# Optimization experiments

Measured on AMD Instinct MI355X. Metric: run time of the kernel, lower is better.

## Reference

```python
import jax, jax.numpy as jnp
import numpy as np

B, BARS, BEATS, FRAC = 64, 16, 4, 8
IN_F = 10 * 47 * 2  # 940
LIN_OUT = 100
BEAT_H = 16
BAR_H = 32


def _p(key, shape, scale=0.05):
    return jax.random.normal(key, shape, dtype=jnp.float32) * scale


def setup_inputs() -> dict:
    key = jax.random.key(0)
    ks = jax.random.split(key, 16)
    return {
        "channels": jax.random.normal(ks[0], (B, BARS, BEATS, FRAC, 10, 2, 47), dtype=jnp.float32),
        "lin_w": _p(ks[1], (LIN_OUT, IN_F)),
        "lin_b": _p(ks[2], (LIN_OUT,)),
        # beats LSTM (unidirectional), PyTorch gate order i,f,g,o
        "b_wih": _p(ks[3], (4 * BEAT_H, LIN_OUT)),
        "b_whh": _p(ks[4], (4 * BEAT_H, BEAT_H)),
        "b_bih": _p(ks[5], (4 * BEAT_H,)),
        "b_bhh": _p(ks[6], (4 * BEAT_H,)),
        # bars LSTM, bidirectional: forward (f_) and reverse (r_) directions
        "f_wih": _p(ks[7], (4 * BAR_H, BEAT_H)),
        "f_whh": _p(ks[8], (4 * BAR_H, BAR_H)),
        "f_bih": _p(ks[9], (4 * BAR_H,)),
        "f_bhh": _p(ks[10], (4 * BAR_H,)),
        "r_wih": _p(ks[11], (4 * BAR_H, BEAT_H)),
        "r_whh": _p(ks[12], (4 * BAR_H, BAR_H)),
        "r_bih": _p(ks[13], (4 * BAR_H,)),
        "r_bhh": _p(ks[14], (4 * BAR_H,)),
    }


def lstm(x, wih, whh, bih, bhh):
    """PyTorch-semantics LSTM, batch_first. x: [N, T, F] -> h_seq [N, T, H]."""
    N = x.shape[0]
    H = whh.shape[1]
    # precompute input contribution for all timesteps
    xg = jnp.einsum('ntf,gf->ntg', x, wih) + (bih + bhh)  # [N, T, 4H]

    def step(carry, xt):
        h, c = carry
        gates = xt + h @ whh.T  # [N, 4H]
        i, f, g, o = jnp.split(gates, 4, axis=-1)
        c = jax.nn.sigmoid(f) * c + jax.nn.sigmoid(i) * jnp.tanh(g)
        h = jax.nn.sigmoid(o) * jnp.tanh(c)
        return (h, c), h

    h0 = jnp.zeros((N, H), x.dtype)
    _, hs = jax.lax.scan(step, (h0, h0), jnp.swapaxes(xg, 0, 1))  # [T, N, H]
    return jnp.swapaxes(hs, 0, 1)


def bilstm(x, f_wih, f_whh, f_bih, f_bhh, r_wih, r_whh, r_bih, r_bhh):
    fwd = lstm(x, f_wih, f_whh, f_bih, f_bhh)
    bwd = jnp.flip(lstm(jnp.flip(x, axis=1), r_wih, r_whh, r_bih, r_bhh), axis=1)
    return jnp.concatenate([fwd, bwd], axis=-1)


def reference(channels, lin_w, lin_b,
              b_wih, b_whh, b_bih, b_bhh,
              f_wih, f_whh, f_bih, f_bhh,
              r_wih, r_whh, r_bih, r_bhh):
    # channels: [B, bars, beats, frac, 10, 2, 47]
    x = jnp.swapaxes(channels, -1, -2)  # [..., 10, 47, 2]
    x = x.reshape(*x.shape[:4], IN_F)   # squash dims 4..6 -> 940
    x = jax.nn.relu(x @ lin_w.T + lin_b)  # [B, bars, beats, frac, 100]

    # Distributed depth=2: fold (B, bars, beats) into batch, seq over frac
    xb = x.reshape(B * BARS * BEATS, FRAC, LIN_OUT)
    beats = lstm(xb, b_wih, b_whh, b_bih, b_bhh)
    beats = beats.reshape(B, BARS, BEATS, FRAC, BEAT_H)

    # last fraction hidden state, then Distributed depth=1 over beats axis
    xl = beats[:, :, :, -1].reshape(B * BARS, BEATS, BEAT_H)
    bars = bilstm(xl, f_wih, f_whh, f_bih, f_bhh, r_wih, r_whh, r_bih, r_bhh)
    bars = bars.reshape(B, BARS, BEATS, 2 * BAR_H)
    return beats, bars
```

## Files before the change

kernel.cpp:

```cpp
#include <hip/hip_runtime.h>
#include <hip/hip_bf16.h>

typedef float f32x4 __attribute__((ext_vector_type(4)));
typedef short bf16x8 __attribute__((ext_vector_type(8)));
typedef short bf16x4 __attribute__((ext_vector_type(4)));

#define MFMA16(a, b, c) __builtin_amdgcn_mfma_f32_16x16x32_bf16(a, b, c, 0, 0, 0)

constexpr int K1  = 940;
constexpr int NP  = 112;
constexpr int OSL = 136;
constexpr int CHE = 14336;
constexpr int CHB = 28672;

__device__ __forceinline__ float sigf(float x) { return 1.f / (1.f + __expf(-x)); }
__device__ __forceinline__ float tanhfast(float x) { return 2.f / (1.f + __expf(-2.f * x)) - 1.f; }

__device__ __forceinline__ short f2b(float x) {
  __hip_bfloat16 b = __float2bfloat16(x);
  return *reinterpret_cast<short*>(&b);
}

__device__ __forceinline__ void gl_lds16(const void* g, void* l) {
  __builtin_amdgcn_global_load_lds(
      (const __attribute__((address_space(1))) unsigned int*)g,
      (__attribute__((address_space(3))) unsigned int*)l, 16, 0, 0);
}

__global__ void prep_kernel(const float* __restrict__ lin_w,
                            const float* __restrict__ b_wih,
                            __hip_bfloat16* __restrict__ w2c,
                            __hip_bfloat16* __restrict__ bw2) {
  int idx = blockIdx.x * 256 + threadIdx.x;
  if (idx < NP * 1024) {
    int n = idx >> 10, k = idx & 1023;
    float v = 0.f;
    if (n < 100 && k < K1) {
      int c10 = k / 94, rem = k - c10 * 94;
      int c2 = rem / 47, c47 = rem - c2 * 47;
      int f = c10 * 94 + c47 * 2 + c2;
      v = lin_w[n * K1 + f];
    }
    int c = k >> 7, kk = k & 127;
    w2c[c * CHE + n * 128 + (kk ^ ((n & 7) << 3))] = __float2bfloat16(v);
  } else {
    int i2 = idx - NP * 1024;
    if (i2 < 64 * 128) {
      int g = i2 >> 7, k = i2 & 127;
      bw2[i2] = __float2bfloat16((k < 100) ? b_wih[g * 100 + k] : 0.f);
    }
  }
}

__global__ __launch_bounds__(256, 2)
void linear_gemm(const float* __restrict__ ch,
                 const __hip_bfloat16* __restrict__ w2c,
                 const float* __restrict__ lin_b,
                 __hip_bfloat16* __restrict__ out1) {
  __shared__ __align__(16) char smem[73728];
  char* As = smem;
  char* Bs = smem + 16384;

  const int tid = threadIdx.x;
  const int w = tid >> 6, lane = tid & 63;
  const int l16 = lane & 15, bq = lane >> 4;
  const int row0 = blockIdx.x * 64 + w * 16;

  float4 rA[8];
  const float4 f40{0.f, 0.f, 0.f, 0.f};
  const int acolf = (lane & 31) * 4;
  const float* asrc = ch + (long)(row0 + (lane >> 5)) * K1 + acolf;
  auto ldA = [&](int c) {
    const float* p = asrc + c * 128;
    if (c < 7) {
#pragma unroll
      for (int j = 0; j < 8; ++j)
        rA[j] = *reinterpret_cast<const float4*>(p + (long)j * 2 * K1);
    } else {
      const bool ok = acolf < 44;
#pragma unroll
      for (int j = 0; j < 8; ++j)
        rA[j] = ok ? *reinterpret_cast<const float4*>(p + (long)j * 2 * K1) : f40;
    }
  };
  auto stA = [&]() {
#pragma unroll
    for (int j = 0; j < 8; ++j) {
      const int row = w * 16 + (lane >> 5) + 2 * j;
      const int byte = row * 256 + (((lane & 31) * 8) ^ ((row & 7) << 4));
      bf16x4 v = {f2b(rA[j].x), f2b(rA[j].y), f2b(rA[j].z), f2b(rA[j].w)};
      *reinterpret_cast<bf16x4*>(As + byte) = v;
    }
  };

  auto dmaB = [&](int c, int buf) {
    const __hip_bfloat16* src = w2c + c * CHE + w * 3584 + lane * 8;
    char* dst = Bs + buf * CHB + w * 7168;
#pragma unroll
    for (int j = 0; j < 7; ++j)
      gl_lds16(src + j * 512, dst + j * 1024);
  };

  ldA(0);
  dmaB(0, 0);
  stA();
  asm volatile("s_waitcnt vmcnt(0) lgkmcnt(0)" ::: "memory");
  __builtin_amdgcn_s_barrier();
  __builtin_amdgcn_sched_barrier(0);

  f32x4 acc[7] = {};
  const int fsw = (l16 & 7) << 4;
  const int abase = (w * 16 + l16) * 256;

#pragma unroll
  for (int c = 0; c < 8; ++c) {
    if (c < 7) {
      ldA(c + 1);
      dmaB(c + 1, (c + 1) & 1);
    }
    const char* Bp = Bs + (c & 1) * CHB;
#pragma unroll
    for (int ks = 0; ks < 4; ++ks) {
      const int ko = (ks * 64 + bq * 16) ^ fsw;
      bf16x8 a = *reinterpret_cast<const bf16x8*>(As + abase + ko);
#pragma unroll
      for (int nt = 0; nt < 7; ++nt) {
        bf16x8 b = *reinterpret_cast<const bf16x8*>(Bp + (nt * 16 + l16) * 256 + ko);
        acc[nt] = MFMA16(a, b, acc[nt]);
      }
    }
    asm volatile("s_waitcnt lgkmcnt(0)" ::: "memory");
    if (c < 7) stA();
    asm volatile("s_waitcnt vmcnt(0) lgkmcnt(0)" ::: "memory");
    __builtin_amdgcn_s_barrier();
    __builtin_amdgcn_sched_barrier(0);
  }

#pragma unroll
  for (int nt = 0; nt < 7; ++nt) {
    const int col = nt * 16 + l16;
    const float bias = (col < 100) ? lin_b[col] : 0.f;
#pragma unroll
    for (int r = 0; r < 4; ++r) {
      float v = (col < 100) ? fmaxf(acc[nt][r] + bias, 0.f) : 0.f;
      out1[(long)(row0 + bq * 4 + r) * 112 + col] = __float2bfloat16(v);
    }
  }
}

__global__ __launch_bounds__(256)
void lstm_kernel(const __hip_bfloat16* __restrict__ out1,
                 const __hip_bfloat16* __restrict__ bw2,
                 const float* __restrict__ bih,
                 const float* __restrict__ bhh,
                 const float* __restrict__ whh,
                 const float* __restrict__ fwih, const float* __restrict__ fwhh,
                 const float* __restrict__ fbih, const float* __restrict__ fbhh,
                 const float* __restrict__ rwih, const float* __restrict__ rwhh,
                 const float* __restrict__ rbih, const float* __restrict__ rbhh,
                 float* __restrict__ beats,
                 float* __restrict__ bars) {
  __shared__ __align__(16) __hip_bfloat16 out_s[64 * OSL];
  __shared__ float xg_s[64 * 65];
  __shared__ float hlast[8][16];
  __shared__ float hb[2][32];
  __shared__ float gact[2][128];

  const int tid = threadIdx.x;
  const int w = tid >> 6, lane = tid & 63;
  const int l16 = lane & 15, bq = lane >> 4;
  const long rbase = (long)blockIdx.x * 64;

#pragma unroll
  for (int it = 0; it < 4; ++it) {
    const int e = it * 256 + tid;
    if (e < 896) {
      const int row = e / 14, g = e - row * 14;
      *reinterpret_cast<bf16x8*>(&out_s[row * OSL + g * 8]) =
          *reinterpret_cast<const bf16x8*>(&out1[(rbase + row) * 112 + g * 8]);
    }
  }
  if (tid < 128) {
    const int row = tid >> 1, c0 = 112 + (tid & 1) * 8;
    bf16x8 z = {0, 0, 0, 0, 0, 0, 0, 0};
    *reinterpret_cast<bf16x8*>(&out_s[row * OSL + c0]) = z;
  }
  __syncthreads();

  {
    bf16x8 av[4];
#pragma unroll
    for (int s = 0; s < 4; ++s)
      av[s] = *reinterpret_cast<const bf16x8*>(&out_s[(w * 16 + l16) * OSL + s * 32 + bq * 8]);
    f32x4 xacc[4] = {};
#pragma unroll
    for (int gt = 0; gt < 4; ++gt) {
#pragma unroll
      for (int s = 0; s < 4; ++s) {
        bf16x8 b = *reinterpret_cast<const bf16x8*>(&bw2[(gt * 16 + l16) * 128 + s * 32 + bq * 8]);
        xacc[gt] = MFMA16(av[s], b, xacc[gt]);
      }
    }
#pragma unroll
    for (int gt = 0; gt < 4; ++gt) {
      const int gate = gt * 16 + l16;
      const float bias = bih[gate] + bhh[gate];
#pragma unroll
      for (int r = 0; r < 4; ++r)
        xg_s[(w * 16 + bq * 4 + r) * 65 + gate] = xacc[gt][r] + bias;
    }
  }

  {
    const int cell = lane & 15;
    float wr[16];
#pragma unroll
    for (int u = 0; u < 16; ++u) wr[u] = whh[lane * 16 + u];
    float xv0[8], xv1[8];
#pragma unroll
    for (int t = 0; t < 8; ++t) {
      xv0[t] = xg_s[(w * 16 + t) * 65 + lane];
      xv1[t] = xg_s[(w * 16 + 8 + t) * 65 + lane];
    }
    float h0[16], h1[16];
#pragma unroll
    for (int u = 0; u < 16; ++u) { h0[u] = 0.f; h1[u] = 0.f; }
    float c0 = 0.f, c1 = 0.f;
    const long sg0 = (long)blockIdx.x * 8 + 2 * w;
    const long sg1 = sg0 + 1;
#pragma unroll
    for (int t = 0; t < 8; ++t) {
      float p0 = xv0[t], p1 = xv1[t];
#pragma unroll
      for (int u = 0; u < 16; ++u) { p0 += wr[u] * h0[u]; p1 += wr[u] * h1[u]; }
      const bool istanh = (lane >= 32 && lane < 48);
      float a0 = istanh ? tanhfast(p0) : sigf(p0);
      float a1 = istanh ? tanhfast(p1) : sigf(p1);
      float gi0 = __shfl(a0, cell),      gi1 = __shfl(a1, cell);
      float gf0 = __shfl(a0, cell + 16), gf1 = __shfl(a1, cell + 16);
      float gg0 = __shfl(a0, cell + 32), gg1 = __shfl(a1, cell + 32);
      float go0 = __shfl(a0, cell + 48), go1 = __shfl(a1, cell + 48);
      c0 = gf0 * c0 + gi0 * gg0;
      c1 = gf1 * c1 + gi1 * gg1;
      float hn0 = go0 * tanhfast(c0);
      float hn1 = go1 * tanhfast(c1);
#pragma unroll
      for (int u = 0; u < 16; ++u) { h0[u] = __shfl(hn0, u); h1[u] = __shfl(hn1, u); }
      if (lane < 16) {
        beats[sg0 * 128 + t * 16 + lane] = hn0;
        beats[sg1 * 128 + t * 16 + lane] = hn1;
        if (t == 7) {
          hlast[2 * w][lane]     = hn0;
          hlast[2 * w + 1][lane] = hn1;
        }
      }
    }
  }
  __syncthreads();

  {
    const int dir = tid >> 7, g = tid & 127;
    const float* wihp = dir ? rwih : fwih;
    const float* whhp = dir ? rwhh : fwhh;
    const float bias = dir ? (rbih[g] + rbhh[g]) : (fbih[g] + fbhh[g]);
    float wi[16], wh[32];
#pragma unroll
    for (int u = 0; u < 16; ++u) wi[u] = wihp[g * 16 + u];
#pragma unroll
    for (int u = 0; u < 32; ++u) wh[u] = whhp[g * 32 + u];
    for (int b2 = 0; b2 < 2; ++b2) {
      const int n = blockIdx.x * 2 + b2;
      float c = 0.f;
      if (g < 32) hb[dir][g] = 0.f;
      __syncthreads();
      for (int t = 0; t < 4; ++t) {
        const int tt = dir ? (3 - t) : t;
        float pre = bias;
#pragma unroll
        for (int u = 0; u < 16; ++u) pre += wi[u] * hlast[b2 * 4 + tt][u];
#pragma unroll
        for (int u = 0; u < 32; ++u) pre += wh[u] * hb[dir][u];
        gact[dir][g] = (g >= 64 && g < 96) ? tanhfast(pre) : sigf(pre);
        __syncthreads();
        if (g < 32) {
          c = gact[dir][32 + g] * c + gact[dir][g] * gact[dir][64 + g];
          float hn = gact[dir][96 + g] * tanhfast(c);
          hb[dir][g] = hn;
          bars[(n * 4 + tt) * 64 + dir * 32 + g] = hn;
        }
        __syncthreads();
      }
    }
  }
}

extern "C" void kernel_launch(void* const* d_in, const int* in_sizes, int n_in,
                              void* d_out, int out_size, void* d_ws, size_t ws_size,
                              hipStream_t stream) {
  const float* ch    = (const float*)d_in[0];
  const float* lin_w = (const float*)d_in[1];
  const float* lin_b = (const float*)d_in[2];
  const float* b_wih = (const float*)d_in[3];
  const float* b_whh = (const float*)d_in[4];
  const float* b_bih = (const float*)d_in[5];
  const float* b_bhh = (const float*)d_in[6];
  const float* f_wih = (const float*)d_in[7];
  const float* f_whh = (const float*)d_in[8];
  const float* f_bih = (const float*)d_in[9];
  const float* f_bhh = (const float*)d_in[10];
  const float* r_wih = (const float*)d_in[11];
  const float* r_whh = (const float*)d_in[12];
  const float* r_bih = (const float*)d_in[13];
  const float* r_bhh = (const float*)d_in[14];

  char* ws = (char*)d_ws;
  __hip_bfloat16* w2c  = (__hip_bfloat16*)ws;
  __hip_bfloat16* bw2  = (__hip_bfloat16*)(ws + 229376);
  __hip_bfloat16* out1 = (__hip_bfloat16*)(ws + 245760);
  float*          out  = (float*)d_out;

  prep_kernel<<<480, 256, 0, stream>>>(lin_w, b_wih, w2c, bw2);
  linear_gemm<<<512, 256, 0, stream>>>(ch, w2c, lin_b, out1);
  lstm_kernel<<<512, 256, 0, stream>>>(out1, bw2, b_bih, b_bhh, b_whh,
                                       f_wih, f_whh, f_bih, f_bhh,
                                       r_wih, r_whh, r_bih, r_bhh,
                                       out, out + 524288);
}
```

Measured before the change: 234.1 us.

## Stream fp32 A tiles via direct-to-LDS DMA with triple-buffered K pipeline

The linear GEMM no longer loads the fp32 activations into registers and converts them to bf16 before storing them to LDS. It now copies the raw fp32 tiles straight into LDS with global_load_lds, in 64-wide K chunks across a triple buffer, and converts to bf16 at fragment-read time. The weight layout is re-chunked to 64-wide K slices and double-buffered, and the wait uses vmcnt(4) so loads stay in flight across iterations. This is meant to cut register pressure and the VALU store path, and to overlap the memory traffic better. In exchange it adds more barriers (15 chunks instead of 8), a conversion inside the inner loop, and a larger LDS footprint.

```diff
diff --git a/kernel.cpp b/kernel.cpp
--- a/kernel.cpp
+++ b/kernel.cpp
@@ -3,15 +3,14 @@
 
 typedef float f32x4 __attribute__((ext_vector_type(4)));
 typedef short bf16x8 __attribute__((ext_vector_type(8)));
-typedef short bf16x4 __attribute__((ext_vector_type(4)));
 
 #define MFMA16(a, b, c) __builtin_amdgcn_mfma_f32_16x16x32_bf16(a, b, c, 0, 0, 0)
 
 constexpr int K1  = 940;
 constexpr int NP  = 112;
 constexpr int OSL = 136;
-constexpr int CHE = 14336;
-constexpr int CHB = 28672;
+constexpr int BCH = 14336;
+constexpr int ACH = 16384;
 
 __device__ __forceinline__ float sigf(float x) { return 1.f / (1.f + __expf(-x)); }
 __device__ __forceinline__ float tanhfast(float x) { return 2.f / (1.f + __expf(-2.f * x)) - 1.f; }
@@ -34,15 +33,17 @@
   int idx = blockIdx.x * 256 + threadIdx.x;
   if (idx < NP * 1024) {
     int n = idx >> 10, k = idx & 1023;
-    float v = 0.f;
-    if (n < 100 && k < K1) {
-      int c10 = k / 94, rem = k - c10 * 94;
-      int c2 = rem / 47, c47 = rem - c2 * 47;
-      int f = c10 * 94 + c47 * 2 + c2;
-      v = lin_w[n * K1 + f];
-    }
-    int c = k >> 7, kk = k & 127;
-    w2c[c * CHE + n * 128 + (kk ^ ((n & 7) << 3))] = __float2bfloat16(v);
+    if (k < 960) {
+      float v = 0.f;
+      if (n < 100 && k < K1) {
+        int c10 = k / 94, rem = k - c10 * 94;
+        int c2 = rem / 47, c47 = rem - c2 * 47;
+        int f = c10 * 94 + c47 * 2 + c2;
+        v = lin_w[n * K1 + f];
+      }
+      int c = k >> 6, kk = k & 63;
+      w2c[c * 7168 + n * 64 + (kk ^ ((n & 7) << 3))] = __float2bfloat16(v);
+    }
   } else {
     int i2 = idx - NP * 1024;
     if (i2 < 64 * 128) {
@@ -57,83 +58,76 @@
                  const __hip_bfloat16* __restrict__ w2c,
                  const float* __restrict__ lin_b,
                  __hip_bfloat16* __restrict__ out1) {
-  __shared__ __align__(16) char smem[73728];
+  __shared__ __align__(16) char smem[3 * ACH + 2 * BCH];
   char* As = smem;
-  char* Bs = smem + 16384;
+  char* Bs = smem + 3 * ACH;
 
   const int tid = threadIdx.x;
   const int w = tid >> 6, lane = tid & 63;
   const int l16 = lane & 15, bq = lane >> 4;
-  const int row0 = blockIdx.x * 64 + w * 16;
-
-  float4 rA[8];
-  const float4 f40{0.f, 0.f, 0.f, 0.f};
-  const int acolf = (lane & 31) * 4;
-  const float* asrc = ch + (long)(row0 + (lane >> 5)) * K1 + acolf;
-  auto ldA = [&](int c) {
-    const float* p = asrc + c * 128;
-    if (c < 7) {
-#pragma unroll
-      for (int j = 0; j < 8; ++j)
-        rA[j] = *reinterpret_cast<const float4*>(p + (long)j * 2 * K1);
-    } else {
-      const bool ok = acolf < 44;
-#pragma unroll
-      for (int j = 0; j < 8; ++j)
-        rA[j] = ok ? *reinterpret_cast<const float4*>(p + (long)j * 2 * K1) : f40;
+  const int row0 = blockIdx.x * 64;
+
+  auto dmaA = [&](int c, int buf) {
+    char* dst = As + buf * ACH + w * 4096;
+#pragma unroll
+    for (int j = 0; j < 4; ++j) {
+      const int row = w * 16 + 4 * j + (lane >> 4);
+      const int inner = ((lane & 15) * 16) ^ ((row & 7) << 4);
+      const char* src = (const char*)ch +
+                        ((long)(row0 + row) * K1 + c * 64) * 4 + inner;
+      if (c == 14 && inner >= 176) src = (const char*)ch;
+      gl_lds16(src, dst + j * 1024);
     }
   };
-  auto stA = [&]() {
-#pragma unroll
-    for (int j = 0; j < 8; ++j) {
-      const int row = w * 16 + (lane >> 5) + 2 * j;
-      const int byte = row * 256 + (((lane & 31) * 8) ^ ((row & 7) << 4));
-      bf16x4 v = {f2b(rA[j].x), f2b(rA[j].y), f2b(rA[j].z), f2b(rA[j].w)};
-      *reinterpret_cast<bf16x4*>(As + byte) = v;
+
+  auto dmaB = [&](int c, int buf) {
+#pragma unroll
+    for (int j = 0; j < 4; ++j) {
+      const int t = w * 4 + j;
+      if (t < 14)
+        gl_lds16((const char*)w2c + c * BCH + t * 1024 + lane * 16,
+                 Bs + buf * BCH + t * 1024);
     }
   };
 
-  auto dmaB = [&](int c, int buf) {
-    const __hip_bfloat16* src = w2c + c * CHE + w * 3584 + lane * 8;
-    char* dst = Bs + buf * CHB + w * 7168;
-#pragma unroll
-    for (int j = 0; j < 7; ++j)
-      gl_lds16(src + j * 512, dst + j * 1024);
-  };
-
-  ldA(0);
   dmaB(0, 0);
-  stA();
-  asm volatile("s_waitcnt vmcnt(0) lgkmcnt(0)" ::: "memory");
+  dmaA(0, 0);
+  dmaA(1, 1);
+  asm volatile("s_waitcnt vmcnt(4)" ::: "memory");
   __builtin_amdgcn_s_barrier();
   __builtin_amdgcn_sched_barrier(0);
 
   f32x4 acc[7] = {};
-  const int fsw = (l16 & 7) << 4;
-  const int abase = (w * 16 + l16) * 256;
-
-#pragma unroll
-  for (int c = 0; c < 8; ++c) {
-    if (c < 7) {
-      ldA(c + 1);
-      dmaB(c + 1, (c + 1) & 1);
-    }
-    const char* Bp = Bs + (c & 1) * CHB;
-#pragma unroll
-    for (int ks = 0; ks < 4; ++ks) {
-      const int ko = (ks * 64 + bq * 16) ^ fsw;
-      bf16x8 a = *reinterpret_cast<const bf16x8*>(As + abase + ko);
+  const int swzA = (l16 & 7) << 4;
+
+#pragma unroll
+  for (int c = 0; c < 15; ++c) {
+    if (c + 1 < 15) dmaB(c + 1, (c + 1) & 1);
+    if (c + 2 < 15) dmaA(c + 2, (c + 2) % 3);
+    const char* Ap = As + (c % 3) * ACH + (w * 16 + l16) * 256;
+    const char* Bp = Bs + (c & 1) * BCH;
+#pragma unroll
+    for (int ks = 0; ks < 2; ++ks) {
+      const int ab = ks * 128 + bq * 32;
+      f32x4 a0 = *reinterpret_cast<const f32x4*>(Ap + (ab ^ swzA));
+      f32x4 a1 = *reinterpret_cast<const f32x4*>(Ap + ((ab + 16) ^ swzA));
+      bf16x8 af = {f2b(a0[0]), f2b(a0[1]), f2b(a0[2]), f2b(a0[3]),
+                   f2b(a1[0]), f2b(a1[1]), f2b(a1[2]), f2b(a1[3])};
 #pragma unroll
       for (int nt = 0; nt < 7; ++nt) {
-        bf16x8 b = *reinterpret_cast<const bf16x8*>(Bp + (nt * 16 + l16) * 256 + ko);
-        acc[nt] = MFMA16(a, b, acc[nt]);
-      }
-    }
-    asm volatile("s_waitcnt lgkmcnt(0)" ::: "memory");
-    if (c < 7) stA();
-    asm volatile("s_waitcnt vmcnt(0) lgkmcnt(0)" ::: "memory");
-    __builtin_amdgcn_s_barrier();
-    __builtin_amdgcn_sched_barrier(0);
+        const int rowb = nt * 16 + l16;
+        bf16x8 b = *reinterpret_cast<const bf16x8*>(
+            Bp + rowb * 128 + ((ks * 64 + bq * 16) ^ ((rowb & 7) << 4)));
+        acc[nt] = MFMA16(af, b, acc[nt]);
+      }
+    }
+    if (c < 14) {
+      asm volatile("s_waitcnt lgkmcnt(0)" ::: "memory");
+      if (c == 13) asm volatile("s_waitcnt vmcnt(0)" ::: "memory");
+      else         asm volatile("s_waitcnt vmcnt(4)" ::: "memory");
+      __builtin_amdgcn_s_barrier();
+      __builtin_amdgcn_sched_barrier(0);
+    }
   }
 
 #pragma unroll
@@ -143,7 +137,7 @@
 #pragma unroll
     for (int r = 0; r < 4; ++r) {
       float v = (col < 100) ? fmaxf(acc[nt][r] + bias, 0.f) : 0.f;
-      out1[(long)(row0 + bq * 4 + r) * 112 + col] = __float2bfloat16(v);
+      out1[(long)(row0 + w * 16 + bq * 4 + r) * 112 + col] = __float2bfloat16(v);
     }
   }
 }
```

Measured after the change: 226.7 us. -3.2%, faster.
